# Kernel tuning notes

Measured on AMD Instinct MI355X. Metric: run time of the kernel, lower is better.

The kernel has to match this reference:

```python
import jax, jax.numpy as jnp
import numpy as np

T, H, I, E, K, R = 16384, 2048, 1024, 8, 2, 16


def setup_inputs() -> dict:
    key = jax.random.key(0)
    ks = jax.random.split(key, 9)
    hidden_states = jax.random.normal(ks[0], (T, H), dtype=jnp.float32)
    tw = jax.random.uniform(ks[1], (T, K), dtype=jnp.float32)
    topk_weights = tw / jnp.sum(tw, axis=-1, keepdims=True)  # renormalized router probs
    topk_ids = jax.random.randint(ks[2], (T, K), 0, E, dtype=jnp.int32)
    s = 0.02  # init scale to keep activations sane
    w13 = jax.random.normal(ks[3], (E, 2 * I, H), dtype=jnp.float32) * s
    w2 = jax.random.normal(ks[4], (E, H, I), dtype=jnp.float32) * s
    gate_up_lora_a = jax.random.normal(ks[5], (E, R, H), dtype=jnp.float32) * s
    gate_up_lora_b = jax.random.normal(ks[6], (E, 2 * I, R), dtype=jnp.float32) * s
    down_lora_a = jax.random.normal(ks[7], (E, R, I), dtype=jnp.float32) * s
    down_lora_b = jax.random.normal(ks[8], (E, H, R), dtype=jnp.float32) * s
    return dict(hidden_states=hidden_states, topk_weights=topk_weights, topk_ids=topk_ids,
                w13=w13, w2=w2,
                gate_up_lora_a=gate_up_lora_a, gate_up_lora_b=gate_up_lora_b,
                down_lora_a=down_lora_a, down_lora_b=down_lora_b)


def reference(hidden_states, topk_weights, topk_ids, w13, w2,
              gate_up_lora_a, gate_up_lora_b, down_lora_a, down_lora_b):
    T_, H_ = hidden_states.shape
    E_ = w13.shape[0]
    I_ = w2.shape[2]
    x = hidden_states
    # Dense [T, E] routing weight matrix from top-k dispatch (scatter-add of router probs).
    rw = jnp.zeros((T_, E_), dtype=x.dtype).at[jnp.arange(T_)[:, None], topk_ids].add(topk_weights)

    def expert_step(acc, inp):
        w13_e, w2_e, a1, b1, a2, b2, rw_e = inp
        # gate_up projection + LoRA delta BEFORE activation
        h = x @ w13_e.T + (x @ a1.T) @ b1.T              # [T, 2I]
        act = jax.nn.silu(h[:, :I_]) * h[:, I_:]         # gated SiLU -> [T, I]
        # down projection + LoRA delta BEFORE final reduction
        y = act @ w2_e.T + (act @ a2.T) @ b2.T           # [T, H]
        return acc + rw_e[:, None] * y, None

    out, _ = jax.lax.scan(
        expert_step, jnp.zeros_like(x),
        (w13, w2, gate_up_lora_a, gate_up_lora_b, down_lora_a, down_lora_b, rw.T))
    return out
```

## Files before the change

### kernel.cpp

```cpp
#include <hip/hip_runtime.h>
#include <hip/hip_bf16.h>

#define T_ 16384
#define H_ 2048
#define I_ 1024
#define E_ 8
#define K_ 2
#define R_ 16
#define P_ (T_*K_)
#define BM 128
#define BK 32

typedef float  f32x4  __attribute__((ext_vector_type(4)));
typedef __bf16 bf16x4 __attribute__((ext_vector_type(4)));
typedef __bf16 bf16x8 __attribute__((ext_vector_type(8)));

__device__ __forceinline__ int swzc(int r, int c) {
  return (c & 7) | ((((c >> 3) ^ ((r >> 1) & 3)) & 3) << 3);
}

__device__ __forceinline__ void cvt4(f32x4 v, bf16x4* h, bf16x4* l) {
#pragma unroll
  for (int j = 0; j < 4; ++j) {
    float f = v[j];
    __bf16 hh = (__bf16)f;
    (*h)[j] = hh;
    (*l)[j] = (__bf16)(f - (float)hh);
  }
}

__global__ __launch_bounds__(256) void zero_kernel(float* __restrict__ out, int* __restrict__ cnt) {
  size_t i = (size_t)blockIdx.x * 256 + threadIdx.x;
  f32x4 z = {0.f, 0.f, 0.f, 0.f};
  if (i < (size_t)T_ * H_ / 4) ((f32x4*)out)[i] = z;
  if (i < E_) cnt[i] = 0;
}

__global__ __launch_bounds__(256) void route_kernel(const int* __restrict__ ids,
                                                    const float* __restrict__ tw,
                                                    int* __restrict__ cnt,
                                                    int* __restrict__ tok,
                                                    float* __restrict__ wgt) {
  int s = blockIdx.x * 256 + threadIdx.x;
  if (s < P_) {
    int e = ids[s];
    int pos = atomicAdd(&cnt[e], 1);
    tok[e * P_ + pos] = s;
    wgt[e * P_ + pos] = tw[s];
  }
}

__global__ __launch_bounds__(256) void lora_u_kernel(const float* __restrict__ x,
                                                     const float* __restrict__ a1,
                                                     const int* __restrict__ ids,
                                                     float* __restrict__ U) {
  int sIdx = blockIdx.x * 4 + (threadIdx.x >> 6);
  int lane = threadIdx.x & 63;
  int t = sIdx >> 1;
  int e = ids[sIdx];
  int r = lane >> 2, part = lane & 3;
  const float* xp = x + (size_t)t * H_;
  const float* ap = a1 + ((size_t)e * R_ + r) * H_;
  float acc = 0.f;
  for (int h0 = part * 4; h0 < H_; h0 += 16) {
    f32x4 xv = *(const f32x4*)(xp + h0);
    f32x4 av = *(const f32x4*)(ap + h0);
    acc += xv[0]*av[0] + xv[1]*av[1] + xv[2]*av[2] + xv[3]*av[3];
  }
  acc += __shfl_xor(acc, 1);
  acc += __shfl_xor(acc, 2);
  if (part == 0) U[(size_t)sIdx * R_ + r] = acc;
}

__global__ __launch_bounds__(256) void lora_v_kernel(const __bf16* __restrict__ acth,
                                                     const __bf16* __restrict__ actl,
                                                     const float* __restrict__ a2,
                                                     const int* __restrict__ ids,
                                                     float* __restrict__ V) {
  int sIdx = blockIdx.x * 4 + (threadIdx.x >> 6);
  int lane = threadIdx.x & 63;
  int e = ids[sIdx];
  int r = lane >> 2, part = lane & 3;
  const __bf16* hp = acth + (size_t)sIdx * I_;
  const __bf16* lp = actl + (size_t)sIdx * I_;
  const float* ap = a2 + ((size_t)e * R_ + r) * I_;
  float acc = 0.f;
  for (int i0 = part * 4; i0 < I_; i0 += 16) {
    bf16x4 hv = *(const bf16x4*)(hp + i0);
    bf16x4 lv = *(const bf16x4*)(lp + i0);
    f32x4 av = *(const f32x4*)(ap + i0);
#pragma unroll
    for (int j = 0; j < 4; ++j) acc += ((float)hv[j] + (float)lv[j]) * av[j];
  }
  acc += __shfl_xor(acc, 1);
  acc += __shfl_xor(acc, 2);
  if (part == 0) V[(size_t)sIdx * R_ + r] = acc;
}

__global__ __launch_bounds__(256, 2) void gemm1_kernel(
    const float* __restrict__ x, const float* __restrict__ w13,
    const float* __restrict__ b1, const float* __restrict__ U,
    const int* __restrict__ cnt, const int* __restrict__ tok,
    __bf16* __restrict__ acth, __bf16* __restrict__ actl) {
  const int e = blockIdx.z;
  const int n = cnt[e];
  const int row0 = blockIdx.y * BM;
  if (row0 >= n) return;
  const int c0 = blockIdx.x * 64;

  __shared__ __bf16 lAh[2][BM*BK], lAl[2][BM*BK], lBh[2][BM*BK], lBl[2][BM*BK];
  __shared__ float sU[BM * R_];
  __shared__ int sTok[BM];

  const int tS = threadIdx.x;
  const int lane = tS & 63, wid = tS >> 6;
  const int wm = (wid & 1) * 64, wn = (wid >> 1) * 32;
  const int lr = lane & 15, lk = lane >> 4;

  const int srow = tS >> 3;
  const int sc4 = (tS & 7) * 4;
  const float* aptr[4];
  const float* bptr[4];
#pragma unroll
  for (int q = 0; q < 4; ++q) {
    int r = srow + q * 32;
    int i = row0 + r; if (i >= n) i = n - 1;
    int s = tok[e * P_ + i];
    aptr[q] = x + (size_t)(s >> 1) * H_ + sc4;
    int bn = (r < 64) ? (c0 + r) : (I_ + c0 + (r - 64));
    bptr[q] = w13 + ((size_t)e * (2 * I_) + bn) * H_ + sc4;
  }

  f32x4 accg[4][2], accu[4][2];
  const f32x4 Z4 = {0.f, 0.f, 0.f, 0.f};
#pragma unroll
  for (int mf = 0; mf < 4; ++mf)
#pragma unroll
    for (int nf = 0; nf < 2; ++nf) { accg[mf][nf] = Z4; accu[mf][nf] = Z4; }

  int arow[4], brow[2];
#pragma unroll
  for (int mf = 0; mf < 4; ++mf) arow[mf] = wm + mf * 16 + lr;
#pragma unroll
  for (int nf = 0; nf < 2; ++nf) brow[nf] = wn + nf * 16 + lr;

  f32x4 ra0[4], rb0[4], ra1[4], rb1[4];

  auto g1_load = [&](f32x4* rA, f32x4* rB, int kof) {
#pragma unroll
    for (int q = 0; q < 4; ++q) {
      rA[q] = *(const f32x4*)(aptr[q] + kof);
      rB[q] = *(const f32x4*)(bptr[q] + kof);
    }
  };
  auto g1_write = [&](int buf, const f32x4* rA, const f32x4* rB) {
#pragma unroll
    for (int q = 0; q < 4; ++q) {
      int r = srow + q * 32; int sc = r * BK + swzc(r, sc4);
      bf16x4 h, l;
      cvt4(rA[q], &h, &l); *(bf16x4*)&lAh[buf][sc] = h; *(bf16x4*)&lAl[buf][sc] = l;
      cvt4(rB[q], &h, &l); *(bf16x4*)&lBh[buf][sc] = h; *(bf16x4*)&lBl[buf][sc] = l;
    }
  };
  auto g1_step = [&](int bs) {
    bf16x8 Ah[4], Al[4], Bh[4], Bl[4];
#pragma unroll
    for (int mf = 0; mf < 4; ++mf) {
      int rr = arow[mf]; int off = rr * BK + ((lk ^ ((rr >> 1) & 3)) << 3);
      Ah[mf] = *(const bf16x8*)&lAh[bs][off];
      Al[mf] = *(const bf16x8*)&lAl[bs][off];
    }
#pragma unroll
    for (int nf = 0; nf < 2; ++nf) {
      int rg = brow[nf]; int og = rg * BK + ((lk ^ ((rg >> 1) & 3)) << 3);
      Bh[nf] = *(const bf16x8*)&lBh[bs][og];
      Bl[nf] = *(const bf16x8*)&lBl[bs][og];
      int ru = 64 + rg; int ou = ru * BK + ((lk ^ ((ru >> 1) & 3)) << 3);
      Bh[2 + nf] = *(const bf16x8*)&lBh[bs][ou];
      Bl[2 + nf] = *(const bf16x8*)&lBl[bs][ou];
    }
#pragma unroll
    for (int mf = 0; mf < 4; ++mf)
#pragma unroll
      for (int nf = 0; nf < 2; ++nf) {
        accg[mf][nf] = __builtin_amdgcn_mfma_f32_16x16x32_bf16(Ah[mf], Bh[nf], accg[mf][nf], 0, 0, 0);
        accg[mf][nf] = __builtin_amdgcn_mfma_f32_16x16x32_bf16(Ah[mf], Bl[nf], accg[mf][nf], 0, 0, 0);
        accg[mf][nf] = __builtin_amdgcn_mfma_f32_16x16x32_bf16(Al[mf], Bh[nf], accg[mf][nf], 0, 0, 0);
        accu[mf][nf] = __builtin_amdgcn_mfma_f32_16x16x32_bf16(Ah[mf], Bh[2+nf], accu[mf][nf], 0, 0, 0);
        accu[mf][nf] = __builtin_amdgcn_mfma_f32_16x16x32_bf16(Ah[mf], Bl[2+nf], accu[mf][nf], 0, 0, 0);
        accu[mf][nf] = __builtin_amdgcn_mfma_f32_16x16x32_bf16(Al[mf], Bh[2+nf], accu[mf][nf], 0, 0, 0);
      }
  };

  const int NK = H_ / BK;
  g1_load(ra0, rb0, 0);
  g1_write(0, ra0, rb0);
  g1_load(ra1, rb1, BK);
  __syncthreads();

  for (int kt = 0; kt < NK; kt += 2) {
    if (kt + 2 < NK) g1_load(ra0, rb0, (kt + 2) * BK);
    g1_step(0);
    g1_write(1, ra1, rb1);
    __syncthreads();
    if (kt + 3 < NK) g1_load(ra1, rb1, (kt + 3) * BK);
    g1_step(1);
    if (kt + 2 < NK) g1_write(0, ra0, rb0);
    __syncthreads();
  }

  if (tS < BM) {
    int i = row0 + tS; if (i >= n) i = n - 1;
    sTok[tS] = tok[e * P_ + i];
  }
  {
    int r2 = tS >> 1, hf = (tS & 1) * 8;
    int i = row0 + r2; if (i >= n) i = n - 1;
    int s = tok[e * P_ + i];
    *(f32x4*)&sU[r2 * R_ + hf]     = *(const f32x4*)&U[(size_t)s * R_ + hf];
    *(f32x4*)&sU[r2 * R_ + hf + 4] = *(const f32x4*)&U[(size_t)s * R_ + hf + 4];
  }
  __syncthreads();

#pragma unroll
  for (int nf = 0; nf < 2; ++nf) {
    int colg = c0 + wn + nf * 16 + lr;
    const float* bg = b1 + ((size_t)e * (2 * I_) + colg) * R_;
    const float* bu = b1 + ((size_t)e * (2 * I_) + I_ + colg) * R_;
    float bgr[R_], bur[R_];
#pragma unroll
    for (int rr = 0; rr < R_; rr += 4) {
      *(f32x4*)&bgr[rr] = *(const f32x4*)(bg + rr);
      *(f32x4*)&bur[rr] = *(const f32x4*)(bu + rr);
    }
#pragma unroll
    for (int mf = 0; mf < 4; ++mf)
#pragma unroll
      for (int j = 0; j < 4; ++j) {
        int trow = wm + mf * 16 + lk * 4 + j;
        float g = accg[mf][nf][j], u = accu[mf][nf][j];
        float ag = 0.f, au = 0.f;
#pragma unroll
        for (int rr = 0; rr < R_; ++rr) { float uv = sU[trow * R_ + rr]; ag += uv * bgr[rr]; au += uv * bur[rr]; }
        g += ag; u += au;
        float a = g / (1.f + __expf(-g)) * u;
        int i = row0 + trow;
        if (i < n) {
          int s = sTok[trow];
          __bf16 hi = (__bf16)a; float hff = (float)hi; __bf16 lo = (__bf16)(a - hff);
          acth[(size_t)s * I_ + colg] = hi;
          actl[(size_t)s * I_ + colg] = lo;
        }
      }
  }
}

__global__ __launch_bounds__(256, 2) void gemm2_kernel(
    const float* __restrict__ w2, const float* __restrict__ b2,
    const __bf16* __restrict__ acth, const __bf16* __restrict__ actl,
    const float* __restrict__ V, const int* __restrict__ cnt,
    const int* __restrict__ tok, const float* __restrict__ wgt,
    float* __restrict__ out) {
  const int e = blockIdx.z;
  const int n = cnt[e];
  const int row0 = blockIdx.y * BM;
  if (row0 >= n) return;
  const int cb0 = blockIdx.x * 128;

  __shared__ __bf16 lAh[2][BM*BK], lAl[2][BM*BK], lBh[2][BM*BK], lBl[2][BM*BK];
  __shared__ float sV[BM * R_];
  __shared__ float sW[BM];
  __shared__ int sTok[BM];

  const int tS = threadIdx.x;
  const int lane = tS & 63, wid = tS >> 6;
  const int wm = (wid & 1) * 64, wn = (wid >> 1) * 64;
  const int lr = lane & 15, lk = lane >> 4;

  const int arow_s = tS >> 1;
  const int acol_s = (tS & 1) * 16;
  const __bf16 *ah_p, *al_p;
  {
    int i = row0 + arow_s; if (i >= n) i = n - 1;
    int s = tok[e * P_ + i];
    ah_p = acth + (size_t)s * I_ + acol_s;
    al_p = actl + (size_t)s * I_ + acol_s;
  }
  const int srow = tS >> 3;
  const int sc4 = (tS & 7) * 4;
  const float* bptr[4];
#pragma unroll
  for (int q = 0; q < 4; ++q) {
    int r = srow + q * 32;
    bptr[q] = w2 + ((size_t)e * H_ + cb0 + r) * I_ + sc4;
  }

  f32x4 acc[4][4];
  const f32x4 Z4 = {0.f, 0.f, 0.f, 0.f};
#pragma unroll
  for (int mf = 0; mf < 4; ++mf)
#pragma unroll
    for (int nf = 0; nf < 4; ++nf) acc[mf][nf] = Z4;

  int arow[4], brow[4];
#pragma unroll
  for (int mf = 0; mf < 4; ++mf) arow[mf] = wm + mf * 16 + lr;
#pragma unroll
  for (int nf = 0; nf < 4; ++nf) brow[nf] = wn + nf * 16 + lr;

  bf16x8 rah0[2], ral0[2], rah1[2], ral1[2];
  f32x4 rb0[4], rb1[4];

  auto g2_load = [&](bf16x8* rh, bf16x8* rl, f32x4* rB, int kof) {
#pragma unroll
    for (int c = 0; c < 2; ++c) {
      rh[c] = *(const bf16x8*)(ah_p + kof + c * 8);
      rl[c] = *(const bf16x8*)(al_p + kof + c * 8);
    }
#pragma unroll
    for (int q = 0; q < 4; ++q) rB[q] = *(const f32x4*)(bptr[q] + kof);
  };
  auto g2_write = [&](int buf, const bf16x8* rh, const bf16x8* rl, const f32x4* rB) {
#pragma unroll
    for (int c = 0; c < 2; ++c) {
      int col = acol_s + c * 8;
      int sc = arow_s * BK + swzc(arow_s, col);
      *(bf16x8*)&lAh[buf][sc] = rh[c]; *(bf16x8*)&lAl[buf][sc] = rl[c];
    }
#pragma unroll
    for (int q = 0; q < 4; ++q) {
      int r = srow + q * 32; int sc = r * BK + swzc(r, sc4);
      bf16x4 h, l; cvt4(rB[q], &h, &l);
      *(bf16x4*)&lBh[buf][sc] = h; *(bf16x4*)&lBl[buf][sc] = l;
    }
  };
  auto g2_step = [&](int bs) {
    bf16x8 Ah[4], Al[4];
#pragma unroll
    for (int mf = 0; mf < 4; ++mf) {
      int rr = arow[mf]; int off = rr * BK + ((lk ^ ((rr >> 1) & 3)) << 3);
      Ah[mf] = *(const bf16x8*)&lAh[bs][off];
      Al[mf] = *(const bf16x8*)&lAl[bs][off];
    }
#pragma unroll
    for (int nf = 0; nf < 4; ++nf) {
      int rr = brow[nf]; int off = rr * BK + ((lk ^ ((rr >> 1) & 3)) << 3);
      bf16x8 Bh = *(const bf16x8*)&lBh[bs][off];
      bf16x8 Bl = *(const bf16x8*)&lBl[bs][off];
#pragma unroll
      for (int mf = 0; mf < 4; ++mf) {
        acc[mf][nf] = __builtin_amdgcn_mfma_f32_16x16x32_bf16(Ah[mf], Bh, acc[mf][nf], 0, 0, 0);
        acc[mf][nf] = __builtin_amdgcn_mfma_f32_16x16x32_bf16(Ah[mf], Bl, acc[mf][nf], 0, 0, 0);
        acc[mf][nf] = __builtin_amdgcn_mfma_f32_16x16x32_bf16(Al[mf], Bh, acc[mf][nf], 0, 0, 0);
      }
    }
  };

  const int NK = I_ / BK;
  g2_load(rah0, ral0, rb0, 0);
  g2_write(0, rah0, ral0, rb0);
  g2_load(rah1, ral1, rb1, BK);
  __syncthreads();

  for (int kt = 0; kt < NK; kt += 2) {
    if (kt + 2 < NK) g2_load(rah0, ral0, rb0, (kt + 2) * BK);
    g2_step(0);
    g2_write(1, rah1, ral1, rb1);
    __syncthreads();
    if (kt + 3 < NK) g2_load(rah1, ral1, rb1, (kt + 3) * BK);
    g2_step(1);
    if (kt + 2 < NK) g2_write(0, rah0, ral0, rb0);
    __syncthreads();
  }

  if (tS < BM) {
    int i = row0 + tS;
    sW[tS] = (i < n) ? wgt[e * P_ + i] : 0.f;
    int ii = (i < n) ? i : (n - 1);
    sTok[tS] = tok[e * P_ + ii];
  }
  {
    int r2 = tS >> 1, hf = (tS & 1) * 8;
    int i = row0 + r2; if (i >= n) i = n - 1;
    int s = tok[e * P_ + i];
    *(f32x4*)&sV[r2 * R_ + hf]     = *(const f32x4*)&V[(size_t)s * R_ + hf];
    *(f32x4*)&sV[r2 * R_ + hf + 4] = *(const f32x4*)&V[(size_t)s * R_ + hf + 4];
  }
  __syncthreads();

#pragma unroll
  for (int nf = 0; nf < 4; ++nf) {
    int col = cb0 + wn + nf * 16 + lr;
    const float* b2p = b2 + ((size_t)e * H_ + col) * R_;
    float br_[R_];
#pragma unroll
    for (int rr = 0; rr < R_; rr += 4) *(f32x4*)&br_[rr] = *(const f32x4*)(b2p + rr);
#pragma unroll
    for (int mf = 0; mf < 4; ++mf)
#pragma unroll
      for (int j = 0; j < 4; ++j) {
        int trow = wm + mf * 16 + lk * 4 + j;
        int i = row0 + trow;
        if (i < n) {
          float y = acc[mf][nf][j];
#pragma unroll
          for (int rr = 0; rr < R_; ++rr) y += sV[trow * R_ + rr] * br_[rr];
          unsafeAtomicAdd(&out[(size_t)(sTok[trow] >> 1) * H_ + col], sW[trow] * y);
        }
      }
  }
}

extern "C" void kernel_launch(void* const* d_in, const int* in_sizes, int n_in,
                              void* d_out, int out_size, void* d_ws, size_t ws_size,
                              hipStream_t stream) {
  const float* x   = (const float*)d_in[0];
  const float* tw  = (const float*)d_in[1];
  const int*   ids = (const int*)d_in[2];
  const float* w13 = (const float*)d_in[3];
  const float* w2  = (const float*)d_in[4];
  const float* a1  = (const float*)d_in[5];
  const float* b1  = (const float*)d_in[6];
  const float* a2  = (const float*)d_in[7];
  const float* b2  = (const float*)d_in[8];
  float* out = (float*)d_out;

  char* ws = (char*)d_ws;
  size_t o = 0;
  int* cnt = (int*)(ws + o);      o += 256;
  int* tok = (int*)(ws + o);      o += (size_t)E_ * P_ * 4;
  float* wgt = (float*)(ws + o);  o += (size_t)E_ * P_ * 4;
  float* U = (float*)(ws + o);    o += (size_t)P_ * R_ * 4;
  float* V = (float*)(ws + o);    o += (size_t)P_ * R_ * 4;
  __bf16* acth = (__bf16*)(ws + o); o += (size_t)P_ * I_ * 2;
  __bf16* actl = (__bf16*)(ws + o); o += (size_t)P_ * I_ * 2;
  if (ws_size < o) return;

  zero_kernel<<<(T_ * H_ / 4 + 255) / 256, 256, 0, stream>>>(out, cnt);
  route_kernel<<<P_ / 256, 256, 0, stream>>>(ids, tw, cnt, tok, wgt);
  lora_u_kernel<<<P_ / 4, 256, 0, stream>>>(x, a1, ids, U);
  gemm1_kernel<<<dim3(I_ / 64, P_ / BM, E_), 256, 0, stream>>>(x, w13, b1, U, cnt, tok, acth, actl);
  lora_v_kernel<<<P_ / 4, 256, 0, stream>>>(acth, actl, a2, ids, V);
  gemm2_kernel<<<dim3(H_ / 128, P_ / BM, E_), 256, 0, stream>>>(w2, b2, acth, actl, V, cnt, tok, wgt, out);
}
```

Before: 2.703 ms.

## Pre-split fp32 inputs and weights into bf16 hi/lo buffers and regroup LoRA kernels

Adds split kernels that convert x, w13 and w2 into bf16 high/low pairs once per call, so the GEMM tiles load bf16 directly instead of converting fp32 inside the k-loop. The LoRA U/V kernels are regrouped per expert so each wave reuses one LoRA-A row across 16 tokens. The grid axes are swapped so row blocks vary fastest. In exchange, whole weight tensors must be written and read again in bf16 pairs, roughly doubling weight traffic before the GEMMs and requiring a much larger workspace, with a fallback path when the workspace is too small.

```diff
diff --git a/kernel.cpp b/kernel.cpp
--- a/kernel.cpp
+++ b/kernel.cpp
@@ -1,5 +1,6 @@
 #include <hip/hip_runtime.h>
 #include <hip/hip_bf16.h>
+#include <type_traits>
 
 #define T_ 16384
 #define H_ 2048
@@ -34,6 +35,18 @@
   f32x4 z = {0.f, 0.f, 0.f, 0.f};
   if (i < (size_t)T_ * H_ / 4) ((f32x4*)out)[i] = z;
   if (i < E_) cnt[i] = 0;
+}
+
+__global__ __launch_bounds__(256) void split_kernel(const float* __restrict__ src,
+                                                    __bf16* __restrict__ dh,
+                                                    __bf16* __restrict__ dl, long n4) {
+  long i = (long)blockIdx.x * 256 + threadIdx.x;
+  if (i < n4) {
+    f32x4 v = ((const f32x4*)src)[i];
+    bf16x4 h, l; cvt4(v, &h, &l);
+    ((bf16x4*)dh)[i] = h;
+    ((bf16x4*)dl)[i] = l;
+  }
 }
 
 __global__ __launch_bounds__(256) void route_kernel(const int* __restrict__ ids,
@@ -52,61 +65,108 @@
 
 __global__ __launch_bounds__(256) void lora_u_kernel(const float* __restrict__ x,
                                                      const float* __restrict__ a1,
-                                                     const int* __restrict__ ids,
+                                                     const int* __restrict__ cnt,
+                                                     const int* __restrict__ tok,
                                                      float* __restrict__ U) {
-  int sIdx = blockIdx.x * 4 + (threadIdx.x >> 6);
-  int lane = threadIdx.x & 63;
-  int t = sIdx >> 1;
-  int e = ids[sIdx];
-  int r = lane >> 2, part = lane & 3;
-  const float* xp = x + (size_t)t * H_;
-  const float* ap = a1 + ((size_t)e * R_ + r) * H_;
-  float acc = 0.f;
-  for (int h0 = part * 4; h0 < H_; h0 += 16) {
-    f32x4 xv = *(const f32x4*)(xp + h0);
-    f32x4 av = *(const f32x4*)(ap + h0);
-    acc += xv[0]*av[0] + xv[1]*av[1] + xv[2]*av[2] + xv[3]*av[3];
-  }
-  acc += __shfl_xor(acc, 1);
-  acc += __shfl_xor(acc, 2);
-  if (part == 0) U[(size_t)sIdx * R_ + r] = acc;
+  const int e = blockIdx.y;
+  const int n = cnt[e];
+  const int i0 = blockIdx.x * 64;
+  if (i0 >= n) return;
+  const int w = threadIdx.x >> 6, lane = threadIdx.x & 63;
+  const int r = lane >> 2, part = lane & 3;
+  const int ib = i0 + w * 16;
+
+  int sp[16];
+  const float* xp[16];
+#pragma unroll
+  for (int p = 0; p < 16; ++p) {
+    int ii = ib + p; if (ii >= n) ii = n - 1;
+    sp[p] = tok[e * P_ + ii];
+    xp[p] = x + (size_t)(sp[p] >> 1) * H_ + part * 4;
+  }
+  const float* ap = a1 + ((size_t)e * R_ + r) * H_ + part * 4;
+
+  float acc[16];
+#pragma unroll
+  for (int p = 0; p < 16; ++p) acc[p] = 0.f;
+
+  for (int h0 = 0; h0 < H_; h0 += 16) {
+    f32x4 a4 = *(const f32x4*)(ap + h0);
+#pragma unroll
+    for (int p = 0; p < 16; ++p) {
+      f32x4 xv = *(const f32x4*)(xp[p] + h0);
+      acc[p] += xv[0]*a4[0] + xv[1]*a4[1] + xv[2]*a4[2] + xv[3]*a4[3];
+    }
+  }
+#pragma unroll
+  for (int p = 0; p < 16; ++p) {
+    acc[p] += __shfl_xor(acc[p], 1);
+    acc[p] += __shfl_xor(acc[p], 2);
+    if (part == 0 && ib + p < n) U[(size_t)sp[p] * R_ + r] = acc[p];
+  }
 }
 
 __global__ __launch_bounds__(256) void lora_v_kernel(const __bf16* __restrict__ acth,
                                                      const __bf16* __restrict__ actl,
                                                      const float* __restrict__ a2,
-                                                     const int* __restrict__ ids,
+                                                     const int* __restrict__ cnt,
+                                                     const int* __restrict__ tok,
                                                      float* __restrict__ V) {
-  int sIdx = blockIdx.x * 4 + (threadIdx.x >> 6);
-  int lane = threadIdx.x & 63;
-  int e = ids[sIdx];
-  int r = lane >> 2, part = lane & 3;
-  const __bf16* hp = acth + (size_t)sIdx * I_;
-  const __bf16* lp = actl + (size_t)sIdx * I_;
-  const float* ap = a2 + ((size_t)e * R_ + r) * I_;
-  float acc = 0.f;
-  for (int i0 = part * 4; i0 < I_; i0 += 16) {
-    bf16x4 hv = *(const bf16x4*)(hp + i0);
-    bf16x4 lv = *(const bf16x4*)(lp + i0);
-    f32x4 av = *(const f32x4*)(ap + i0);
-#pragma unroll
-    for (int j = 0; j < 4; ++j) acc += ((float)hv[j] + (float)lv[j]) * av[j];
-  }
-  acc += __shfl_xor(acc, 1);
-  acc += __shfl_xor(acc, 2);
-  if (part == 0) V[(size_t)sIdx * R_ + r] = acc;
-}
-
+  const int e = blockIdx.y;
+  const int n = cnt[e];
+  const int i0 = blockIdx.x * 64;
+  if (i0 >= n) return;
+  const int w = threadIdx.x >> 6, lane = threadIdx.x & 63;
+  const int r = lane >> 2, part = lane & 3;
+  const int ib = i0 + w * 16;
+
+  int sp[16];
+#pragma unroll
+  for (int p = 0; p < 16; ++p) {
+    int ii = ib + p; if (ii >= n) ii = n - 1;
+    sp[p] = tok[e * P_ + ii];
+  }
+  const float* ap = a2 + ((size_t)e * R_ + r) * I_ + part * 4;
+
+  float acc[16];
+#pragma unroll
+  for (int p = 0; p < 16; ++p) acc[p] = 0.f;
+
+  for (int i1 = 0; i1 < I_; i1 += 16) {
+    f32x4 a4 = *(const f32x4*)(ap + i1);
+#pragma unroll
+    for (int p = 0; p < 16; ++p) {
+      size_t off = (size_t)sp[p] * I_ + i1 + part * 4;
+      bf16x4 hv = *(const bf16x4*)(acth + off);
+      bf16x4 lv = *(const bf16x4*)(actl + off);
+#pragma unroll
+      for (int j = 0; j < 4; ++j) acc[p] += ((float)hv[j] + (float)lv[j]) * a4[j];
+    }
+  }
+#pragma unroll
+  for (int p = 0; p < 16; ++p) {
+    acc[p] += __shfl_xor(acc[p], 1);
+    acc[p] += __shfl_xor(acc[p], 2);
+    if (part == 0 && ib + p < n) V[(size_t)sp[p] * R_ + r] = acc[p];
+  }
+}
+
+struct S1g { bf16x8 ah[2], al[2], bh[2], bl[2]; };
+struct S0g { f32x4 a[4], b[4]; };
+
+template<int MODE>
 __global__ __launch_bounds__(256, 2) void gemm1_kernel(
     const float* __restrict__ x, const float* __restrict__ w13,
+    const __bf16* __restrict__ xh, const __bf16* __restrict__ xl,
+    const __bf16* __restrict__ w13h, const __bf16* __restrict__ w13l,
     const float* __restrict__ b1, const float* __restrict__ U,
     const int* __restrict__ cnt, const int* __restrict__ tok,
     __bf16* __restrict__ acth, __bf16* __restrict__ actl) {
   const int e = blockIdx.z;
   const int n = cnt[e];
-  const int row0 = blockIdx.y * BM;
+  const int row0 = blockIdx.x * BM;
   if (row0 >= n) return;
-  const int c0 = blockIdx.x * 64;
+  const int c0 = blockIdx.y * 64;
 
   __shared__ __bf16 lAh[2][BM*BK], lAl[2][BM*BK], lBh[2][BM*BK], lBl[2][BM*BK];
   __shared__ float sU[BM * R_];
@@ -117,18 +177,18 @@
   const int wm = (wid & 1) * 64, wn = (wid >> 1) * 32;
   const int lr = lane & 15, lk = lane >> 4;
 
-  const int srow = tS >> 3;
-  const int sc4 = (tS & 7) * 4;
-  const float* aptr[4];
-  const float* bptr[4];
-#pragma unroll
-  for (int q = 0; q < 4; ++q) {
-    int r = srow + q * 32;
-    int i = row0 + r; if (i >= n) i = n - 1;
+  const int ar = tS >> 1;
+  const int c8 = (tS & 1) * 16;
+  const __bf16 *Ah_p = nullptr, *Al_p = nullptr, *Bh_p = nullptr, *Bl_p = nullptr;
+  const float *Af_p = nullptr, *Bf_p = nullptr;
+  {
+    int i = row0 + ar; if (i >= n) i = n - 1;
     int s = tok[e * P_ + i];
-    aptr[q] = x + (size_t)(s >> 1) * H_ + sc4;
-    int bn = (r < 64) ? (c0 + r) : (I_ + c0 + (r - 64));
-    bptr[q] = w13 + ((size_t)e * (2 * I_) + bn) * H_ + sc4;
+    size_t axo = (size_t)(s >> 1) * H_ + c8;
+    int bn = (ar < 64) ? (c0 + ar) : (I_ + c0 + (ar - 64));
+    size_t bxo = ((size_t)e * (2 * I_) + bn) * H_ + c8;
+    if constexpr (MODE) { Ah_p = xh + axo; Al_p = xl + axo; Bh_p = w13h + bxo; Bl_p = w13l + bxo; }
+    else { Af_p = x + axo; Bf_p = w13 + bxo; }
   }
 
   f32x4 accg[4][2], accu[4][2];
@@ -144,25 +204,47 @@
 #pragma unroll
   for (int nf = 0; nf < 2; ++nf) brow[nf] = wn + nf * 16 + lr;
 
-  f32x4 ra0[4], rb0[4], ra1[4], rb1[4];
-
-  auto g1_load = [&](f32x4* rA, f32x4* rB, int kof) {
-#pragma unroll
-    for (int q = 0; q < 4; ++q) {
-      rA[q] = *(const f32x4*)(aptr[q] + kof);
-      rB[q] = *(const f32x4*)(bptr[q] + kof);
+  using SS = std::conditional_t<MODE != 0, S1g, S0g>;
+  SS sA, sB;
+
+  auto LD = [&](auto& rp, int kof) {
+    if constexpr (MODE) {
+#pragma unroll
+      for (int j = 0; j < 2; ++j) {
+        rp.ah[j] = *(const bf16x8*)(Ah_p + kof + j * 8);
+        rp.al[j] = *(const bf16x8*)(Al_p + kof + j * 8);
+        rp.bh[j] = *(const bf16x8*)(Bh_p + kof + j * 8);
+        rp.bl[j] = *(const bf16x8*)(Bl_p + kof + j * 8);
+      }
+    } else {
+#pragma unroll
+      for (int j = 0; j < 4; ++j) {
+        rp.a[j] = *(const f32x4*)(Af_p + kof + j * 4);
+        rp.b[j] = *(const f32x4*)(Bf_p + kof + j * 4);
+      }
     }
   };
-  auto g1_write = [&](int buf, const f32x4* rA, const f32x4* rB) {
-#pragma unroll
-    for (int q = 0; q < 4; ++q) {
-      int r = srow + q * 32; int sc = r * BK + swzc(r, sc4);
-      bf16x4 h, l;
-      cvt4(rA[q], &h, &l); *(bf16x4*)&lAh[buf][sc] = h; *(bf16x4*)&lAl[buf][sc] = l;
-      cvt4(rB[q], &h, &l); *(bf16x4*)&lBh[buf][sc] = h; *(bf16x4*)&lBl[buf][sc] = l;
+  auto WR = [&](int buf, auto& rp) {
+    if constexpr (MODE) {
+#pragma unroll
+      for (int j = 0; j < 2; ++j) {
+        int sc = ar * BK + swzc(ar, c8 + j * 8);
+        *(bf16x8*)&lAh[buf][sc] = rp.ah[j];
+        *(bf16x8*)&lAl[buf][sc] = rp.al[j];
+        *(bf16x8*)&lBh[buf][sc] = rp.bh[j];
+        *(bf16x8*)&lBl[buf][sc] = rp.bl[j];
+      }
+    } else {
+#pragma unroll
+      for (int j = 0; j < 4; ++j) {
+        int sc = ar * BK + swzc(ar, c8 + j * 4);
+        bf16x4 h, l;
+        cvt4(rp.a[j], &h, &l); *(bf16x4*)&lAh[buf][sc] = h; *(bf16x4*)&lAl[buf][sc] = l;
+        cvt4(rp.b[j], &h, &l); *(bf16x4*)&lBh[buf][sc] = h; *(bf16x4*)&lBl[buf][sc] = l;
+      }
     }
   };
-  auto g1_step = [&](int bs) {
+  auto STEP = [&](int bs) {
     bf16x8 Ah[4], Al[4], Bh[4], Bl[4];
 #pragma unroll
     for (int mf = 0; mf < 4; ++mf) {
@@ -193,19 +275,16 @@
   };
 
   const int NK = H_ / BK;
-  g1_load(ra0, rb0, 0);
-  g1_write(0, ra0, rb0);
-  g1_load(ra1, rb1, BK);
+  LD(sA, 0); WR(0, sA); LD(sB, BK);
   __syncthreads();
-
   for (int kt = 0; kt < NK; kt += 2) {
-    if (kt + 2 < NK) g1_load(ra0, rb0, (kt + 2) * BK);
-    g1_step(0);
-    g1_write(1, ra1, rb1);
+    if (kt + 2 < NK) LD(sA, (kt + 2) * BK);
+    STEP(0);
+    WR(1, sB);
     __syncthreads();
-    if (kt + 3 < NK) g1_load(ra1, rb1, (kt + 3) * BK);
-    g1_step(1);
-    if (kt + 2 < NK) g1_write(0, ra0, rb0);
+    if (kt + 3 < NK) LD(sB, (kt + 3) * BK);
+    STEP(1);
+    if (kt + 2 < NK) WR(0, sA);
     __syncthreads();
   }
 
@@ -255,17 +334,23 @@
   }
 }
 
+struct S2_1 { bf16x8 ah[2], al[2], bh[2], bl[2]; };
+struct S2_0 { bf16x8 ah[2], al[2]; f32x4 b[4]; };
+
+template<int MODE>
 __global__ __launch_bounds__(256, 2) void gemm2_kernel(
-    const float* __restrict__ w2, const float* __restrict__ b2,
+    const float* __restrict__ w2,
+    const __bf16* __restrict__ w2h, const __bf16* __restrict__ w2l,
+    const float* __restrict__ b2,
     const __bf16* __restrict__ acth, const __bf16* __restrict__ actl,
     const float* __restrict__ V, const int* __restrict__ cnt,
     const int* __restrict__ tok, const float* __restrict__ wgt,
     float* __restrict__ out) {
   const int e = blockIdx.z;
   const int n = cnt[e];
-  const int row0 = blockIdx.y * BM;
+  const int row0 = blockIdx.x * BM;
   if (row0 >= n) return;
-  const int cb0 = blockIdx.x * 128;
+  const int cb0 = blockIdx.y * 128;
 
   __shared__ __bf16 lAh[2][BM*BK], lAl[2][BM*BK], lBh[2][BM*BK], lBl[2][BM*BK];
   __shared__ float sV[BM * R_];
@@ -277,22 +362,19 @@
   const int wm = (wid & 1) * 64, wn = (wid >> 1) * 64;
   const int lr = lane & 15, lk = lane >> 4;
 
-  const int arow_s = tS >> 1;
-  const int acol_s = (tS & 1) * 16;
+  const int ar = tS >> 1;
+  const int c8 = (tS & 1) * 16;
   const __bf16 *ah_p, *al_p;
+  const __bf16 *Bh_p = nullptr, *Bl_p = nullptr;
+  const float *Bf_p = nullptr;
   {
-    int i = row0 + arow_s; if (i >= n) i = n - 1;
+    int i = row0 + ar; if (i >= n) i = n - 1;
     int s = tok[e * P_ + i];
-    ah_p = acth + (size_t)s * I_ + acol_s;
-    al_p = actl + (size_t)s * I_ + acol_s;
-  }
-  const int srow = tS >> 3;
-  const int sc4 = (tS & 7) * 4;
-  const float* bptr[4];
-#pragma unroll
-  for (int q = 0; q < 4; ++q) {
-    int r = srow + q * 32;
-    bptr[q] = w2 + ((size_t)e * H_ + cb0 + r) * I_ + sc4;
+    ah_p = acth + (size_t)s * I_ + c8;
+    al_p = actl + (size_t)s * I_ + c8;
+    size_t bxo = ((size_t)e * H_ + cb0 + ar) * I_ + c8;
+    if constexpr (MODE) { Bh_p = w2h + bxo; Bl_p = w2l + bxo; }
+    else { Bf_p = w2 + bxo; }
   }
 
   f32x4 acc[4][4];
@@ -308,33 +390,50 @@
 #pragma unroll
   for (int nf = 0; nf < 4; ++nf) brow[nf] = wn + nf * 16 + lr;
 
-  bf16x8 rah0[2], ral0[2], rah1[2], ral1[2];
-  f32x4 rb0[4], rb1[4];
-
-  auto g2_load = [&](bf16x8* rh, bf16x8* rl, f32x4* rB, int kof) {
-#pragma unroll
-    for (int c = 0; c < 2; ++c) {
-      rh[c] = *(const bf16x8*)(ah_p + kof + c * 8);
-      rl[c] = *(const bf16x8*)(al_p + kof + c * 8);
-    }
-#pragma unroll
-    for (int q = 0; q < 4; ++q) rB[q] = *(const f32x4*)(bptr[q] + kof);
+  using SS = std::conditional_t<MODE != 0, S2_1, S2_0>;
+  SS sA, sB;
+
+  auto LD = [&](auto& rp, int kof) {
+#pragma unroll
+    for (int j = 0; j < 2; ++j) {
+      rp.ah[j] = *(const bf16x8*)(ah_p + kof + j * 8);
+      rp.al[j] = *(const bf16x8*)(al_p + kof + j * 8);
+    }
+    if constexpr (MODE) {
+#pragma unroll
+      for (int j = 0; j < 2; ++j) {
+        rp.bh[j] = *(const bf16x8*)(Bh_p + kof + j * 8);
+        rp.bl[j] = *(const bf16x8*)(Bl_p + kof + j * 8);
+      }
+    } else {
+#pragma unroll
+      for (int j = 0; j < 4; ++j) rp.b[j] = *(const f32x4*)(Bf_p + kof + j * 4);
+    }
   };
-  auto g2_write = [&](int buf, const bf16x8* rh, const bf16x8* rl, const f32x4* rB) {
-#pragma unroll
-    for (int c = 0; c < 2; ++c) {
-      int col = acol_s + c * 8;
-      int sc = arow_s * BK + swzc(arow_s, col);
-      *(bf16x8*)&lAh[buf][sc] = rh[c]; *(bf16x8*)&lAl[buf][sc] = rl[c];
-    }
-#pragma unroll
-    for (int q = 0; q < 4; ++q) {
-      int r = srow + q * 32; int sc = r * BK + swzc(r, sc4);
-      bf16x4 h, l; cvt4(rB[q], &h, &l);
-      *(bf16x4*)&lBh[buf][sc] = h; *(bf16x4*)&lBl[buf][sc] = l;
+  auto WR = [&](int buf, auto& rp) {
+#pragma unroll
+    for (int j = 0; j < 2; ++j) {
+      int sc = ar * BK + swzc(ar, c8 + j * 8);
+      *(bf16x8*)&lAh[buf][sc] = rp.ah[j];
+      *(bf16x8*)&lAl[buf][sc] = rp.al[j];
+    }
+    if constexpr (MODE) {
+#pragma unroll
+      for (int j = 0; j < 2; ++j) {
+        int sc = ar * BK + swzc(ar, c8 + j * 8);
+        *(bf16x8*)&lBh[buf][sc] = rp.bh[j];
+        *(bf16x8*)&lBl[buf][sc] = rp.bl[j];
+      }
+    } else {
+#pragma unroll
+      for (int j = 0; j < 4; ++j) {
+        int sc = ar * BK + swzc(ar, c8 + j * 4);
+        bf16x4 h, l; cvt4(rp.b[j], &h, &l);
+        *(bf16x4*)&lBh[buf][sc] = h; *(bf16x4*)&lBl[buf][sc] = l;
+      }
     }
   };
-  auto g2_step = [&](int bs) {
+  auto STEP = [&](int bs) {
     bf16x8 Ah[4], Al[4];
 #pragma unroll
     for (int mf = 0; mf < 4; ++mf) {
@@ -357,19 +456,16 @@
   };
 
   const int NK = I_ / BK;
-  g2_load(rah0, ral0, rb0, 0);
-  g2_write(0, rah0, ral0, rb0);
-  g2_load(rah1, ral1, rb1, BK);
+  LD(sA, 0); WR(0, sA); LD(sB, BK);
   __syncthreads();
-
   for (int kt = 0; kt < NK; kt += 2) {
-    if (kt + 2 < NK) g2_load(rah0, ral0, rb0, (kt + 2) * BK);
-    g2_step(0);
-    g2_write(1, rah1, ral1, rb1);
+    if (kt + 2 < NK) LD(sA, (kt + 2) * BK);
+    STEP(0);
+    WR(1, sB);
     __syncthreads();
-    if (kt + 3 < NK) g2_load(rah1, ral1, rb1, (kt + 3) * BK);
-    g2_step(1);
-    if (kt + 2 < NK) g2_write(0, rah0, ral0, rb0);
+    if (kt + 3 < NK) LD(sB, (kt + 3) * BK);
+    STEP(1);
+    if (kt + 2 < NK) WR(0, sA);
     __syncthreads();
   }
 
@@ -427,19 +523,59 @@
 
   char* ws = (char*)d_ws;
   size_t o = 0;
-  int* cnt = (int*)(ws + o);      o += 256;
-  int* tok = (int*)(ws + o);      o += (size_t)E_ * P_ * 4;
-  float* wgt = (float*)(ws + o);  o += (size_t)E_ * P_ * 4;
-  float* U = (float*)(ws + o);    o += (size_t)P_ * R_ * 4;
-  float* V = (float*)(ws + o);    o += (size_t)P_ * R_ * 4;
-  __bf16* acth = (__bf16*)(ws + o); o += (size_t)P_ * I_ * 2;
-  __bf16* actl = (__bf16*)(ws + o); o += (size_t)P_ * I_ * 2;
-  if (ws_size < o) return;
+  auto alloc = [&](size_t bytes) { size_t p = o; o = (o + bytes + 255) & ~(size_t)255; return p; };
+  size_t o_cnt = alloc(256);
+  size_t o_tok = alloc((size_t)E_ * P_ * 4);
+  size_t o_wgt = alloc((size_t)E_ * P_ * 4);
+  size_t o_U   = alloc((size_t)P_ * R_ * 4);
+  size_t o_V   = alloc((size_t)P_ * R_ * 4);
+  size_t o_ah  = alloc((size_t)P_ * I_ * 2);
+  size_t o_al  = alloc((size_t)P_ * I_ * 2);
+  size_t need_base = o;
+  size_t o_xh  = alloc((size_t)T_ * H_ * 2);
+  size_t o_xl  = alloc((size_t)T_ * H_ * 2);
+  size_t o_wh  = alloc((size_t)E_ * 2 * I_ * H_ * 2);
+  size_t o_wl  = alloc((size_t)E_ * 2 * I_ * H_ * 2);
+  size_t o_2h  = alloc((size_t)E_ * H_ * I_ * 2);
+  size_t o_2l  = alloc((size_t)E_ * H_ * I_ * 2);
+  size_t need_split = o;
+
+  if (ws_size < need_base) return;
+  const bool use_split = (ws_size >= need_split);
+
+  int* cnt   = (int*)(ws + o_cnt);
+  int* tok   = (int*)(ws + o_tok);
+  float* wgt = (float*)(ws + o_wgt);
+  float* U   = (float*)(ws + o_U);
+  float* V   = (float*)(ws + o_V);
+  __bf16* acth = (__bf16*)(ws + o_ah);
+  __bf16* actl = (__bf16*)(ws + o_al);
+  __bf16* xh = (__bf16*)(ws + o_xh),  *xl = (__bf16*)(ws + o_xl);
+  __bf16* wh = (__bf16*)(ws + o_wh),  *wl = (__bf16*)(ws + o_wl);
+  __bf16* w2h = (__bf16*)(ws + o_2h), *w2l = (__bf16*)(ws + o_2l);
 
   zero_kernel<<<(T_ * H_ / 4 + 255) / 256, 256, 0, stream>>>(out, cnt);
   route_kernel<<<P_ / 256, 256, 0, stream>>>(ids, tw, cnt, tok, wgt);
-  lora_u_kernel<<<P_ / 4, 256, 0, stream>>>(x, a1, ids, U);
-  gemm1_kernel<<<dim3(I_ / 64, P_ / BM, E_), 256, 0, stream>>>(x, w13, b1, U, cnt, tok, acth, actl);
-  lora_v_kernel<<<P_ / 4, 256, 0, stream>>>(acth, actl, a2, ids, V);
-  gemm2_kernel<<<dim3(H_ / 128, P_ / BM, E_), 256, 0, stream>>>(w2, b2, acth, actl, V, cnt, tok, wgt, out);
-}
+  if (use_split) {
+    long nx = (long)T_ * H_ / 4, nw = (long)E_ * 2 * I_ * H_ / 4, n2 = (long)E_ * H_ * I_ / 4;
+    split_kernel<<<(nx + 255) / 256, 256, 0, stream>>>(x, xh, xl, nx);
+    split_kernel<<<(nw + 255) / 256, 256, 0, stream>>>(w13, wh, wl, nw);
+    split_kernel<<<(n2 + 255) / 256, 256, 0, stream>>>(w2, w2h, w2l, n2);
+  }
+  lora_u_kernel<<<dim3(P_ / 64, E_), 256, 0, stream>>>(x, a1, cnt, tok, U);
+  if (use_split) {
+    gemm1_kernel<1><<<dim3(P_ / BM, I_ / 64, E_), 256, 0, stream>>>(
+        x, w13, xh, xl, wh, wl, b1, U, cnt, tok, acth, actl);
+  } else {
+    gemm1_kernel<0><<<dim3(P_ / BM, I_ / 64, E_), 256, 0, stream>>>(
+        x, w13, nullptr, nullptr, nullptr, nullptr, b1, U, cnt, tok, acth, actl);
+  }
+  lora_v_kernel<<<dim3(P_ / 64, E_), 256, 0, stream>>>(acth, actl, a2, cnt, tok, V);
+  if (use_split) {
+    gemm2_kernel<1><<<dim3(P_ / BM, H_ / 128, E_), 256, 0, stream>>>(
+        w2, w2h, w2l, b2, acth, actl, V, cnt, tok, wgt, out);
+  } else {
+    gemm2_kernel<0><<<dim3(P_ / BM, H_ / 128, E_), 256, 0, stream>>>(
+        w2, nullptr, nullptr, b2, acth, actl, V, cnt, tok, wgt, out);
+  }
+}
```

Measured after the change: 3.315 ms. +22.7%, slower.

## Single-buffer GEMM LDS for higher occupancy and batch LoRA projections per expert

Applied to the files above, without the earlier changes.

The gemm1 and gemm2 kernels drop their double-buffered LDS tiles in favor of one buffer with extra barriers, and raise launch bounds from 2 to 3 blocks per SM. The aim is to fit more resident waves so latency is hidden by occupancy rather than in-block buffering. The LoRA U and V kernels are regrouped by expert, so each wave reuses one loaded A-row slice across 16 routed slots instead of reloading it per slot. The risks are that the extra __syncthreads serialize global-to-LDS writes against MFMA work, and that the tighter register budget may cause spills.

```diff
diff --git a/kernel.cpp b/kernel.cpp
--- a/kernel.cpp
+++ b/kernel.cpp
@@ -52,52 +52,93 @@
 
 __global__ __launch_bounds__(256) void lora_u_kernel(const float* __restrict__ x,
                                                      const float* __restrict__ a1,
-                                                     const int* __restrict__ ids,
+                                                     const int* __restrict__ cnt,
+                                                     const int* __restrict__ tok,
                                                      float* __restrict__ U) {
-  int sIdx = blockIdx.x * 4 + (threadIdx.x >> 6);
-  int lane = threadIdx.x & 63;
-  int t = sIdx >> 1;
-  int e = ids[sIdx];
-  int r = lane >> 2, part = lane & 3;
-  const float* xp = x + (size_t)t * H_;
-  const float* ap = a1 + ((size_t)e * R_ + r) * H_;
-  float acc = 0.f;
-  for (int h0 = part * 4; h0 < H_; h0 += 16) {
-    f32x4 xv = *(const f32x4*)(xp + h0);
-    f32x4 av = *(const f32x4*)(ap + h0);
-    acc += xv[0]*av[0] + xv[1]*av[1] + xv[2]*av[2] + xv[3]*av[3];
-  }
-  acc += __shfl_xor(acc, 1);
-  acc += __shfl_xor(acc, 2);
-  if (part == 0) U[(size_t)sIdx * R_ + r] = acc;
+  const int e = blockIdx.y;
+  const int n = cnt[e];
+  const int i0 = blockIdx.x * 64;
+  if (i0 >= n) return;
+  const int w = threadIdx.x >> 6, lane = threadIdx.x & 63;
+  const int r = lane >> 2, part = lane & 3;
+  const int ib = i0 + w * 16;
+
+  int sp[16];
+  const float* xp[16];
+#pragma unroll
+  for (int p = 0; p < 16; ++p) {
+    int ii = ib + p; if (ii >= n) ii = n - 1;
+    sp[p] = tok[e * P_ + ii];
+    xp[p] = x + (size_t)(sp[p] >> 1) * H_ + part * 4;
+  }
+  const float* ap = a1 + ((size_t)e * R_ + r) * H_ + part * 4;
+
+  float acc[16];
+#pragma unroll
+  for (int p = 0; p < 16; ++p) acc[p] = 0.f;
+
+  for (int h0 = 0; h0 < H_; h0 += 16) {
+    f32x4 a4 = *(const f32x4*)(ap + h0);
+#pragma unroll
+    for (int p = 0; p < 16; ++p) {
+      f32x4 xv = *(const f32x4*)(xp[p] + h0);
+      acc[p] += xv[0]*a4[0] + xv[1]*a4[1] + xv[2]*a4[2] + xv[3]*a4[3];
+    }
+  }
+#pragma unroll
+  for (int p = 0; p < 16; ++p) {
+    acc[p] += __shfl_xor(acc[p], 1);
+    acc[p] += __shfl_xor(acc[p], 2);
+    if (part == 0 && ib + p < n) U[(size_t)sp[p] * R_ + r] = acc[p];
+  }
 }
 
 __global__ __launch_bounds__(256) void lora_v_kernel(const __bf16* __restrict__ acth,
                                                      const __bf16* __restrict__ actl,
                                                      const float* __restrict__ a2,
-                                                     const int* __restrict__ ids,
+                                                     const int* __restrict__ cnt,
+                                                     const int* __restrict__ tok,
                                                      float* __restrict__ V) {
-  int sIdx = blockIdx.x * 4 + (threadIdx.x >> 6);
-  int lane = threadIdx.x & 63;
-  int e = ids[sIdx];
-  int r = lane >> 2, part = lane & 3;
-  const __bf16* hp = acth + (size_t)sIdx * I_;
-  const __bf16* lp = actl + (size_t)sIdx * I_;
-  const float* ap = a2 + ((size_t)e * R_ + r) * I_;
-  float acc = 0.f;
-  for (int i0 = part * 4; i0 < I_; i0 += 16) {
-    bf16x4 hv = *(const bf16x4*)(hp + i0);
-    bf16x4 lv = *(const bf16x4*)(lp + i0);
-    f32x4 av = *(const f32x4*)(ap + i0);
-#pragma unroll
-    for (int j = 0; j < 4; ++j) acc += ((float)hv[j] + (float)lv[j]) * av[j];
-  }
-  acc += __shfl_xor(acc, 1);
-  acc += __shfl_xor(acc, 2);
-  if (part == 0) V[(size_t)sIdx * R_ + r] = acc;
-}
-
-__global__ __launch_bounds__(256, 2) void gemm1_kernel(
+  const int e = blockIdx.y;
+  const int n = cnt[e];
+  const int i0 = blockIdx.x * 64;
+  if (i0 >= n) return;
+  const int w = threadIdx.x >> 6, lane = threadIdx.x & 63;
+  const int r = lane >> 2, part = lane & 3;
+  const int ib = i0 + w * 16;
+
+  int sp[16];
+#pragma unroll
+  for (int p = 0; p < 16; ++p) {
+    int ii = ib + p; if (ii >= n) ii = n - 1;
+    sp[p] = tok[e * P_ + ii];
+  }
+  const float* ap = a2 + ((size_t)e * R_ + r) * I_ + part * 4;
+
+  float acc[16];
+#pragma unroll
+  for (int p = 0; p < 16; ++p) acc[p] = 0.f;
+
+  for (int i1 = 0; i1 < I_; i1 += 16) {
+    f32x4 a4 = *(const f32x4*)(ap + i1);
+#pragma unroll
+    for (int p = 0; p < 16; ++p) {
+      size_t off = (size_t)sp[p] * I_ + i1 + part * 4;
+      bf16x4 hv = *(const bf16x4*)(acth + off);
+      bf16x4 lv = *(const bf16x4*)(actl + off);
+#pragma unroll
+      for (int j = 0; j < 4; ++j) acc[p] += ((float)hv[j] + (float)lv[j]) * a4[j];
+    }
+  }
+#pragma unroll
+  for (int p = 0; p < 16; ++p) {
+    acc[p] += __shfl_xor(acc[p], 1);
+    acc[p] += __shfl_xor(acc[p], 2);
+    if (part == 0 && ib + p < n) V[(size_t)sp[p] * R_ + r] = acc[p];
+  }
+}
+
+__global__ __launch_bounds__(256, 3) void gemm1_kernel(
     const float* __restrict__ x, const float* __restrict__ w13,
     const float* __restrict__ b1, const float* __restrict__ U,
     const int* __restrict__ cnt, const int* __restrict__ tok,
@@ -108,7 +149,7 @@
   if (row0 >= n) return;
   const int c0 = blockIdx.x * 64;
 
-  __shared__ __bf16 lAh[2][BM*BK], lAl[2][BM*BK], lBh[2][BM*BK], lBl[2][BM*BK];
+  __shared__ __bf16 lAh[BM*BK], lAl[BM*BK], lBh[BM*BK], lBl[BM*BK];
   __shared__ float sU[BM * R_];
   __shared__ int sTok[BM];
 
@@ -153,31 +194,31 @@
       rB[q] = *(const f32x4*)(bptr[q] + kof);
     }
   };
-  auto g1_write = [&](int buf, const f32x4* rA, const f32x4* rB) {
+  auto g1_write = [&](const f32x4* rA, const f32x4* rB) {
 #pragma unroll
     for (int q = 0; q < 4; ++q) {
       int r = srow + q * 32; int sc = r * BK + swzc(r, sc4);
       bf16x4 h, l;
-      cvt4(rA[q], &h, &l); *(bf16x4*)&lAh[buf][sc] = h; *(bf16x4*)&lAl[buf][sc] = l;
-      cvt4(rB[q], &h, &l); *(bf16x4*)&lBh[buf][sc] = h; *(bf16x4*)&lBl[buf][sc] = l;
-    }
-  };
-  auto g1_step = [&](int bs) {
+      cvt4(rA[q], &h, &l); *(bf16x4*)&lAh[sc] = h; *(bf16x4*)&lAl[sc] = l;
+      cvt4(rB[q], &h, &l); *(bf16x4*)&lBh[sc] = h; *(bf16x4*)&lBl[sc] = l;
+    }
+  };
+  auto g1_step = [&]() {
     bf16x8 Ah[4], Al[4], Bh[4], Bl[4];
 #pragma unroll
     for (int mf = 0; mf < 4; ++mf) {
       int rr = arow[mf]; int off = rr * BK + ((lk ^ ((rr >> 1) & 3)) << 3);
-      Ah[mf] = *(const bf16x8*)&lAh[bs][off];
-      Al[mf] = *(const bf16x8*)&lAl[bs][off];
+      Ah[mf] = *(const bf16x8*)&lAh[off];
+      Al[mf] = *(const bf16x8*)&lAl[off];
     }
 #pragma unroll
     for (int nf = 0; nf < 2; ++nf) {
       int rg = brow[nf]; int og = rg * BK + ((lk ^ ((rg >> 1) & 3)) << 3);
-      Bh[nf] = *(const bf16x8*)&lBh[bs][og];
-      Bl[nf] = *(const bf16x8*)&lBl[bs][og];
+      Bh[nf] = *(const bf16x8*)&lBh[og];
+      Bl[nf] = *(const bf16x8*)&lBl[og];
       int ru = 64 + rg; int ou = ru * BK + ((lk ^ ((ru >> 1) & 3)) << 3);
-      Bh[2 + nf] = *(const bf16x8*)&lBh[bs][ou];
-      Bl[2 + nf] = *(const bf16x8*)&lBl[bs][ou];
+      Bh[2 + nf] = *(const bf16x8*)&lBh[ou];
+      Bl[2 + nf] = *(const bf16x8*)&lBl[ou];
     }
 #pragma unroll
     for (int mf = 0; mf < 4; ++mf)
@@ -194,18 +235,20 @@
 
   const int NK = H_ / BK;
   g1_load(ra0, rb0, 0);
-  g1_write(0, ra0, rb0);
+  g1_write(ra0, rb0);
   g1_load(ra1, rb1, BK);
   __syncthreads();
 
   for (int kt = 0; kt < NK; kt += 2) {
     if (kt + 2 < NK) g1_load(ra0, rb0, (kt + 2) * BK);
-    g1_step(0);
-    g1_write(1, ra1, rb1);
+    g1_step();
+    __syncthreads();
+    if (kt + 1 < NK) g1_write(ra1, rb1);
     __syncthreads();
     if (kt + 3 < NK) g1_load(ra1, rb1, (kt + 3) * BK);
-    g1_step(1);
-    if (kt + 2 < NK) g1_write(0, ra0, rb0);
+    g1_step();
+    __syncthreads();
+    if (kt + 2 < NK) g1_write(ra0, rb0);
     __syncthreads();
   }
 
@@ -255,7 +298,7 @@
   }
 }
 
-__global__ __launch_bounds__(256, 2) void gemm2_kernel(
+__global__ __launch_bounds__(256, 3) void gemm2_kernel(
     const float* __restrict__ w2, const float* __restrict__ b2,
     const __bf16* __restrict__ acth, const __bf16* __restrict__ actl,
     const float* __restrict__ V, const int* __restrict__ cnt,
@@ -267,7 +310,7 @@
   if (row0 >= n) return;
   const int cb0 = blockIdx.x * 128;
 
-  __shared__ __bf16 lAh[2][BM*BK], lAl[2][BM*BK], lBh[2][BM*BK], lBl[2][BM*BK];
+  __shared__ __bf16 lAh[BM*BK], lAl[BM*BK], lBh[BM*BK], lBl[BM*BK];
   __shared__ float sV[BM * R_];
   __shared__ float sW[BM];
   __shared__ int sTok[BM];
@@ -320,33 +363,33 @@
 #pragma unroll
     for (int q = 0; q < 4; ++q) rB[q] = *(const f32x4*)(bptr[q] + kof);
   };
-  auto g2_write = [&](int buf, const bf16x8* rh, const bf16x8* rl, const f32x4* rB) {
+  auto g2_write = [&](const bf16x8* rh, const bf16x8* rl, const f32x4* rB) {
 #pragma unroll
     for (int c = 0; c < 2; ++c) {
       int col = acol_s + c * 8;
       int sc = arow_s * BK + swzc(arow_s, col);
-      *(bf16x8*)&lAh[buf][sc] = rh[c]; *(bf16x8*)&lAl[buf][sc] = rl[c];
+      *(bf16x8*)&lAh[sc] = rh[c]; *(bf16x8*)&lAl[sc] = rl[c];
     }
 #pragma unroll
     for (int q = 0; q < 4; ++q) {
       int r = srow + q * 32; int sc = r * BK + swzc(r, sc4);
       bf16x4 h, l; cvt4(rB[q], &h, &l);
-      *(bf16x4*)&lBh[buf][sc] = h; *(bf16x4*)&lBl[buf][sc] = l;
-    }
-  };
-  auto g2_step = [&](int bs) {
+      *(bf16x4*)&lBh[sc] = h; *(bf16x4*)&lBl[sc] = l;
+    }
+  };
+  auto g2_step = [&]() {
     bf16x8 Ah[4], Al[4];
 #pragma unroll
     for (int mf = 0; mf < 4; ++mf) {
       int rr = arow[mf]; int off = rr * BK + ((lk ^ ((rr >> 1) & 3)) << 3);
-      Ah[mf] = *(const bf16x8*)&lAh[bs][off];
-      Al[mf] = *(const bf16x8*)&lAl[bs][off];
+      Ah[mf] = *(const bf16x8*)&lAh[off];
+      Al[mf] = *(const bf16x8*)&lAl[off];
     }
 #pragma unroll
     for (int nf = 0; nf < 4; ++nf) {
       int rr = brow[nf]; int off = rr * BK + ((lk ^ ((rr >> 1) & 3)) << 3);
-      bf16x8 Bh = *(const bf16x8*)&lBh[bs][off];
-      bf16x8 Bl = *(const bf16x8*)&lBl[bs][off];
+      bf16x8 Bh = *(const bf16x8*)&lBh[off];
+      bf16x8 Bl = *(const bf16x8*)&lBl[off];
 #pragma unroll
       for (int mf = 0; mf < 4; ++mf) {
         acc[mf][nf] = __builtin_amdgcn_mfma_f32_16x16x32_bf16(Ah[mf], Bh, acc[mf][nf], 0, 0, 0);
@@ -358,18 +401,20 @@
 
   const int NK = I_ / BK;
   g2_load(rah0, ral0, rb0, 0);
-  g2_write(0, rah0, ral0, rb0);
+  g2_write(rah0, ral0, rb0);
   g2_load(rah1, ral1, rb1, BK);
   __syncthreads();
 
   for (int kt = 0; kt < NK; kt += 2) {
     if (kt + 2 < NK) g2_load(rah0, ral0, rb0, (kt + 2) * BK);
-    g2_step(0);
-    g2_write(1, rah1, ral1, rb1);
+    g2_step();
+    __syncthreads();
+    if (kt + 1 < NK) g2_write(rah1, ral1, rb1);
     __syncthreads();
     if (kt + 3 < NK) g2_load(rah1, ral1, rb1, (kt + 3) * BK);
-    g2_step(1);
-    if (kt + 2 < NK) g2_write(0, rah0, ral0, rb0);
+    g2_step();
+    __syncthreads();
+    if (kt + 2 < NK) g2_write(rah0, ral0, rb0);
     __syncthreads();
   }
 
@@ -438,8 +483,8 @@
 
   zero_kernel<<<(T_ * H_ / 4 + 255) / 256, 256, 0, stream>>>(out, cnt);
   route_kernel<<<P_ / 256, 256, 0, stream>>>(ids, tw, cnt, tok, wgt);
-  lora_u_kernel<<<P_ / 4, 256, 0, stream>>>(x, a1, ids, U);
+  lora_u_kernel<<<dim3(P_ / 64, E_), 256, 0, stream>>>(x, a1, cnt, tok, U);
   gemm1_kernel<<<dim3(I_ / 64, P_ / BM, E_), 256, 0, stream>>>(x, w13, b1, U, cnt, tok, acth, actl);
-  lora_v_kernel<<<P_ / 4, 256, 0, stream>>>(acth, actl, a2, ids, V);
+  lora_v_kernel<<<dim3(P_ / 64, E_), 256, 0, stream>>>(acth, actl, a2, cnt, tok, V);
   gemm2_kernel<<<dim3(H_ / 128, P_ / BM, E_), 256, 0, stream>>>(w2, b2, acth, actl, V, cnt, tok, wgt, out);
 }
```

After: 6.690 ms. 2.48x slower.
